# Performance work log

Hardware: AMD Instinct MI355X
Metric: run time of the kernel (lower is better)

## Reference

```python
import jax, jax.numpy as jnp
import numpy as np

B = 64
D_IN = 4000            # reduced from hardcoded 40000 to fit memory budget (see notes)
N_NODES = 200
ADJ = N_NODES * N_NODES  # 40000 entries per adjacency
E_PER = ADJ // 4         # strictly > 0.75-quantile of 40000 continuous values == top 10000
NEG_SLOPE = 0.2          # GATv2Conv default leaky_relu slope
LN_EPS = 1e-5


def _gelu(x):
    return jax.nn.gelu(x, approximate=False)  # torch F.gelu default = exact erf


def _gatv2(x, src, dst, valid, Wl, bl, Wr, br, att, bias, heads, ch, concat, n):
    # PyG GATv2Conv (share_weights=False): xl = lin_l(x), xr = lin_r(x)
    xl = (x @ Wl + bl).reshape(n, heads, ch)
    xr = (x @ Wr + br).reshape(n, heads, ch)
    e = jax.nn.leaky_relu(xl[src] + xr[dst], NEG_SLOPE)        # [E,H,C]
    logits = jnp.einsum('ehc,hc->eh', e, att)                   # [E,H]
    if valid is not None:
        logits = jnp.where(valid[:, None], logits, -jnp.inf)
    m = jax.ops.segment_max(logits, dst, num_segments=n)
    m = jnp.where(jnp.isfinite(m), m, 0.0)
    ex = jnp.exp(logits - m[dst])
    if valid is not None:
        ex = jnp.where(valid[:, None], ex, 0.0)
    denom = jax.ops.segment_sum(ex, dst, num_segments=n)
    alpha = ex / (denom[dst] + 1e-16)                            # scatter-softmax per target
    out = jax.ops.segment_sum(xl[src] * alpha[..., None], dst, num_segments=n)
    out = out.reshape(n, heads * ch) if concat else out.mean(axis=1)
    return out + bias


def _forward(raw_fc, gbW, gbb, feW1, feb1, feW2, feb2, ln_g, ln_b,
             W1l, b1l, W1r, b1r, att1, bias1,
             W2l, b2l, W2r, b2r, att2, bias2,
             W3l, b3l, W3r, b3r, att3, bias3):
    b = raw_fc.shape[0]
    n = b * N_NODES
    # ---- build_graph ----
    adj = jax.nn.sigmoid(raw_fc @ gbW + gbb).reshape(b, N_NODES, N_NODES)
    adj = (adj + jnp.swapaxes(adj, 1, 2)) * 0.5
    means = adj.mean(axis=2)                    # [B,200]
    stds = jnp.std(adj, axis=2, ddof=1) + 1e-6  # torch std is unbiased
    base = jnp.stack([means, stds], axis=-1).reshape(n, 2)
    h = _gelu(base @ feW1 + feb1) @ feW2 + feb2
    mu = h.mean(-1, keepdims=True)
    var = h.var(-1, keepdims=True)
    x = (h - mu) / jnp.sqrt(var + LN_EPS) * ln_g + ln_b          # LayerNorm(16)
    _, idx = jax.lax.top_k(adj.reshape(b, ADJ), E_PER)           # [B, 10000]
    row = idx // N_NODES
    col = idx % N_NODES
    offs = (jnp.arange(b) * N_NODES)[:, None]
    src = (row + offs).reshape(-1)
    dst = (col + offs).reshape(-1)
    # ---- GAT stack (eval mode: dropout = identity) ----
    x = _gelu(_gatv2(x, src, dst, None, W1l, b1l, W1r, b1r, att1, bias1, 8, 128, True, n))
    # layers 2/3 have add_self_loops=True: remove existing self loops, append one per node
    loops = jnp.arange(n)
    src2 = jnp.concatenate([src, loops])
    dst2 = jnp.concatenate([dst, loops])
    valid2 = jnp.concatenate([src != dst, jnp.ones((n,), bool)])
    x = _gelu(_gatv2(x, src2, dst2, valid2, W2l, b2l, W2r, b2r, att2, bias2, 4, 256, True, n))
    x = _gelu(_gatv2(x, src2, dst2, valid2, W3l, b3l, W3r, b3r, att3, bias3, 1, 512, False, n))
    # global_mean_pool: exactly 200 nodes per graph, contiguous ordering
    return x.reshape(b, N_NODES, 512).mean(axis=1)


def setup_inputs() -> dict:
    key = jax.random.key(0)
    ks = jax.random.split(key, 16)
    f32 = jnp.float32
    def gl(k, shape, fan_in):
        return jax.random.normal(k, shape, f32) / np.sqrt(fan_in)
    inp = {}
    inp['raw_fc'] = jax.random.normal(ks[0], (B, D_IN), f32)
    inp['gbW'] = gl(ks[1], (D_IN, ADJ), D_IN)
    inp['gbb'] = jnp.zeros((ADJ,), f32)
    inp['feW1'] = gl(ks[2], (2, 8), 2);      inp['feb1'] = jnp.zeros((8,), f32)
    inp['feW2'] = gl(ks[3], (8, 16), 8);     inp['feb2'] = jnp.zeros((16,), f32)
    inp['ln_g'] = jnp.ones((16,), f32);      inp['ln_b'] = jnp.zeros((16,), f32)
    inp['W1l'] = gl(ks[4], (16, 8 * 128), 16);   inp['b1l'] = jnp.zeros((8 * 128,), f32)
    inp['W1r'] = gl(ks[5], (16, 8 * 128), 16);   inp['b1r'] = jnp.zeros((8 * 128,), f32)
    inp['att1'] = gl(ks[6], (8, 128), 128);      inp['bias1'] = jnp.zeros((8 * 128,), f32)
    inp['W2l'] = gl(ks[7], (1024, 4 * 256), 1024); inp['b2l'] = jnp.zeros((4 * 256,), f32)
    inp['W2r'] = gl(ks[8], (1024, 4 * 256), 1024); inp['b2r'] = jnp.zeros((4 * 256,), f32)
    inp['att2'] = gl(ks[9], (4, 256), 256);        inp['bias2'] = jnp.zeros((4 * 256,), f32)
    inp['W3l'] = gl(ks[10], (1024, 512), 1024);    inp['b3l'] = jnp.zeros((512,), f32)
    inp['W3r'] = gl(ks[11], (1024, 512), 1024);    inp['b3r'] = jnp.zeros((512,), f32)
    inp['att3'] = gl(ks[12], (1, 512), 512);       inp['bias3'] = jnp.zeros((512,), f32)
    return inp


def reference(raw_fc, gbW, gbb, feW1, feb1, feW2, feb2, ln_g, ln_b,
              W1l, b1l, W1r, b1r, att1, bias1,
              W2l, b2l, W2r, b2r, att2, bias2,
              W3l, b3l, W3r, b3r, att3, bias3):
    return _forward(raw_fc, gbW, gbb, feW1, feb1, feW2, feb2, ln_g, ln_b,
                    W1l, b1l, W1r, b1r, att1, bias1,
                    W2l, b2l, W2r, b2r, att2, bias2,
                    W3l, b3l, W3r, b3r, att3, bias3)
```

## Files before the change

### kernel.cpp

```cpp
#include <hip/hip_runtime.h>
#include <hip/hip_fp16.h>
#include <math.h>
#include <cstdint>
#include <cstddef>

#define NGRAPH 64
#define NN 200
#define ADJN 40000
#define DIN 4000
#define NNODE 12800

typedef float    f32x4 __attribute__((ext_vector_type(4)));
typedef _Float16 f16x8 __attribute__((ext_vector_type(8)));
typedef _Float16 f16x4 __attribute__((ext_vector_type(4)));
typedef _Float16 f16x2 __attribute__((ext_vector_type(2)));
typedef short    bf8v  __attribute__((ext_vector_type(8)));
typedef short    bf4v  __attribute__((ext_vector_type(4)));

union BF8U  { bf8v v; bf4v h[2]; };
union F16X8U{ f16x8 v; f16x4 h[2]; f16x2 p[4]; };

__device__ __forceinline__ unsigned short f2bf(float f) {
  unsigned u = __float_as_uint(f);
  return (unsigned short)((u + 0x7fffu + ((u >> 16) & 1u)) >> 16);
}
__device__ __forceinline__ float bf2f(unsigned short s) {
  return __uint_as_float(((unsigned)s) << 16);
}
__device__ __forceinline__ float gelu_f(float x) {
  return x * 0.5f * (1.0f + erff(x * 0.70710678118654752f));
}

#if defined(__has_builtin)
#if __has_builtin(__builtin_amdgcn_fdot2)
#define FDOT2(a, b, c) __builtin_amdgcn_fdot2((a), (b), (c), false)
#endif
#endif
#ifndef FDOT2
#define FDOT2(a, b, c) ((c) + (float)(a)[0] * (float)(b)[0] + (float)(a)[1] * (float)(b)[1])
#endif

__device__ __forceinline__ void glds16(const _Float16* g, _Float16* l) {
  __builtin_amdgcn_global_load_lds(
      (const __attribute__((address_space(1))) void*)g,
      (__attribute__((address_space(3))) void*)l, 16, 0, 0);
}

__global__ __launch_bounds__(256) void prep_A(const float* __restrict__ A,
                                              short* __restrict__ Ahi,
                                              short* __restrict__ Alo) {
  const int i = blockIdx.x * 256 + threadIdx.x;
  const float v = A[i];
  const unsigned short h = f2bf(v);
  Ahi[i] = (short)h;
  Alo[i] = (short)f2bf(v - bf2f(h));
}

__global__ __launch_bounds__(256) void transp_all(
    const float* __restrict__ W2l, const float* __restrict__ W2r,
    const float* __restrict__ W3l, const float* __restrict__ W3r,
    _Float16* __restrict__ T2l, _Float16* __restrict__ T2r,
    _Float16* __restrict__ T3l, _Float16* __restrict__ T3r) {
  __shared__ float tile[32][33];
  const int z = blockIdx.z;
  if (z >= 2 && blockIdx.y >= 16) return;
  const float* src = (z == 0) ? W2l : (z == 1) ? W2r : (z == 2) ? W3l : W3r;
  _Float16* dst = (z == 0) ? T2l : (z == 1) ? T2r : (z == 2) ? T3l : T3r;
  const int N = (z < 2) ? 1024 : 512;
  const int K = 1024;
  const int bk = blockIdx.x * 32, bn = blockIdx.y * 32;
  const int tx = threadIdx.x & 31, ty = threadIdx.x >> 5;
#pragma unroll
  for (int r = 0; r < 32; r += 8) tile[ty + r][tx] = src[(size_t)(bk + ty + r) * N + bn + tx];
  __syncthreads();
#pragma unroll
  for (int r = 0; r < 32; r += 8)
    dst[(size_t)(bn + ty + r) * K + bk + tx] = (_Float16)tile[tx][ty + r];
}

#define BA_LOADW(WV, K0)                                                        \
  _Pragma("unroll") for (int q = 0; q < 8; ++q)                                 \
    WV[q] = W[(size_t)((K0) + kgrp * 8 + q) * ADJN + n0 + nn];

#define BA_CONV(PB, WV)                                                         \
  { bf4v h0, h1, l0, l1;                                                        \
    _Pragma("unroll") for (int i = 0; i < 4; ++i) {                             \
      unsigned short hh = (unsigned short)(__float_as_uint(WV[i]) >> 16);       \
      h0[i] = (short)hh;                                                        \
      l0[i] = (short)f2bf(WV[i] - bf2f(hh));                                    \
    }                                                                           \
    _Pragma("unroll") for (int i = 0; i < 4; ++i) {                             \
      unsigned short hh = (unsigned short)(__float_as_uint(WV[4 + i]) >> 16);   \
      h1[i] = (short)hh;                                                        \
      l1[i] = (short)f2bf(WV[4 + i] - bf2f(hh));                                \
    }                                                                           \
    *(bf4v*)(Wh[PB] + nn * 44 + kgrp * 8)     = h0;                             \
    *(bf4v*)(Wh[PB] + nn * 44 + kgrp * 8 + 4) = h1;                             \
    *(bf4v*)(Wl[PB] + nn * 44 + kgrp * 8)     = l0;                             \
    *(bf4v*)(Wl[PB] + nn * 44 + kgrp * 8 + 4) = l1;                             \
  }

#define BA_MFMA(PB, AHC, ALC)                                                   \
  _Pragma("unroll") for (int j = 0; j < 4; ++j) {                               \
    const int bc = (j * 16 + (lane & 15)) * 44 + kb;                            \
    BF8U bh, bl;                                                                \
    bh.h[0] = *(const bf4v*)(Wh[PB] + bc);                                      \
    bh.h[1] = *(const bf4v*)(Wh[PB] + bc + 4);                                  \
    bl.h[0] = *(const bf4v*)(Wl[PB] + bc);                                      \
    bl.h[1] = *(const bf4v*)(Wl[PB] + bc + 4);                                  \
    acc[j] = __builtin_amdgcn_mfma_f32_16x16x32_bf16(AHC, bh.v, acc[j], 0, 0, 0); \
    acc[j] = __builtin_amdgcn_mfma_f32_16x16x32_bf16(AHC, bl.v, acc[j], 0, 0, 0); \
    acc[j] = __builtin_amdgcn_mfma_f32_16x16x32_bf16(ALC, bh.v, acc[j], 0, 0, 0); \
  }

#define BA_LOADA(AH, AL, K0)                                                    \
  AH = *(const bf8v*)(Ahi + (size_t)arow * DIN + (K0) + kb);                    \
  AL = *(const bf8v*)(Alo + (size_t)arow * DIN + (K0) + kb);

__global__ __launch_bounds__(256) void build_adj(
    const short* __restrict__ Ahi, const short* __restrict__ Alo,
    const float* __restrict__ W, const float* __restrict__ bias,
    float* __restrict__ adj) {
  __shared__ short Wh[2][64 * 44], Wl[2][64 * 44];
  const int t = threadIdx.x, wave = t >> 6, lane = t & 63;
  const int n0 = blockIdx.x * 64;
  const int nn = t & 63, kgrp = t >> 6;
  const int kb = (lane >> 4) * 8;
  const int arow = wave * 16 + (lane & 15);
  f32x4 acc[4] = {};
  float wva[8], wvb[8];
  bf8v ahs0, als0, ahs1, als1;
  BA_LOADW(wva, 0)
  BA_LOADA(ahs0, als0, 0)
  BA_LOADW(wvb, 32)
  BA_LOADA(ahs1, als1, 32)
  BA_CONV(0, wva)
  for (int it = 0; it < 124; it += 2) {
    __syncthreads();
    {
      const bf8v ahc = ahs0, alc = als0;
      if (it + 2 < 125) {
        const int k2 = (it + 2) * 32;
        BA_LOADW(wva, k2)
        BA_LOADA(ahs0, als0, k2)
      }
      BA_MFMA(0, ahc, alc)
      BA_CONV(1, wvb)
    }
    __syncthreads();
    {
      const bf8v ahc = ahs1, alc = als1;
      if (it + 3 < 125) {
        const int k2 = (it + 3) * 32;
        BA_LOADW(wvb, k2)
        BA_LOADA(ahs1, als1, k2)
      }
      BA_MFMA(1, ahc, alc)
      if (it + 2 < 125) BA_CONV(0, wva)
    }
  }
  __syncthreads();
  BA_MFMA(0, ahs0, als0)
#pragma unroll
  for (int j = 0; j < 4; ++j) {
    const int col = n0 + j * 16 + (lane & 15);
    const float bb = bias[col];
#pragma unroll
    for (int vv = 0; vv < 4; ++vv) {
      const int row = wave * 16 + (lane >> 4) * 4 + vv;
      float x = acc[j][vv] + bb;
      adj[(size_t)row * ADJN + col] = 1.0f / (1.0f + __expf(-x));
    }
  }
}

__global__ __launch_bounds__(256) void symmetrize(const float* __restrict__ adj,
                                                  float* __restrict__ adjS) {
  __shared__ float tl[64][65];
  const int g = blockIdx.x;
  const int i0 = (blockIdx.y >> 2) * 64, j0 = (blockIdx.y & 3) * 64;
  const int tx = threadIdx.x & 63, ty = threadIdx.x >> 6;
  const float* ag = adj + (size_t)g * ADJN;
#pragma unroll
  for (int r = 0; r < 64; r += 4) {
    const int jr = j0 + ty + r;
    tl[ty + r][tx] = (jr < NN && i0 + tx < NN) ? ag[jr * NN + i0 + tx] : 0.f;
  }
  __syncthreads();
#pragma unroll
  for (int r = 0; r < 64; r += 4) {
    const int i = i0 + ty + r, j = j0 + tx;
    if (i < NN && j < NN)
      adjS[(size_t)g * ADJN + i * NN + j] = 0.5f * (ag[i * NN + j] + tl[tx][ty + r]);
  }
}

__global__ __launch_bounds__(256) void rowstats(const float* __restrict__ adjS,
                                                float* __restrict__ meanv,
                                                float* __restrict__ stdv) {
  const int row = blockIdx.x * 4 + (threadIdx.x >> 6);
  const int lane = threadIdx.x & 63;
  const float* r = adjS + (size_t)row * NN;
  float s = 0.f, q = 0.f;
#pragma unroll
  for (int k = 0; k < 4; ++k) {
    int i = k * 64 + lane;
    if (i < NN) { float v = r[i]; s += v; q += v * v; }
  }
#pragma unroll
  for (int off = 32; off > 0; off >>= 1) { s += __shfl_xor(s, off); q += __shfl_xor(q, off); }
  if (lane == 0) {
    float m = s * (1.0f / 200.0f);
    float var = (q - 200.0f * m * m) * (1.0f / 199.0f);
    var = fmaxf(var, 0.f);
    meanv[row] = m;
    stdv[row] = sqrtf(var) + 1e-6f;
  }
}

__global__ __launch_bounds__(1024) void radix_lists(
    const float* __restrict__ adjS,
    int* __restrict__ cnt1, int* __restrict__ cnt2,
    unsigned char* __restrict__ list1, unsigned char* __restrict__ list2) {
  __shared__ unsigned hist[4 * 2048];
  __shared__ unsigned s_pref, s_cA;
  const int g = blockIdx.x, t = threadIdx.x, lane = t & 63, wave = t >> 6;
  const float* v = adjS + (size_t)g * ADJN;
  unsigned prefix = 0, pmask = 0, cA = 0;
  const int shifts[3] = {20, 9, 0};
  const int widths[3] = {2048, 2048, 512};
  for (int pass = 0; pass < 3; ++pass) {
    const int nb = widths[pass], sh = shifts[pass];
    for (int i = t; i < 8192; i += 1024) hist[i] = 0u;
    __syncthreads();
    const int cpy = (lane & 3) * 2048;
    for (int e = t; e < ADJN; e += 1024) {
      unsigned u = __float_as_uint(v[e]);
      if ((u & pmask) == prefix) atomicAdd(&hist[cpy + ((u >> sh) & (nb - 1))], 1u);
    }
    __syncthreads();
    if (t < 64) {
      const int CH = nb >> 6;
      unsigned lsum = 0;
      for (int i = 0; i < CH; ++i) {
        const int b = t * CH + i;
        lsum += hist[b] + hist[2048 + b] + hist[4096 + b] + hist[6144 + b];
      }
      unsigned s = lsum;
#pragma unroll
      for (int off = 1; off < 64; off <<= 1) {
        unsigned o = __shfl_down(s, off);
        if (lane + off < 64) s += o;
      }
      const unsigned need = 10000u - cA;
      unsigned sn = __shfl_down(s, 1);
      const unsigned snext = (lane == 63) ? 0u : sn;
      if (s >= need && snext < need) {
        unsigned cum = snext;
        int bsel = t * CH;
        for (int i = CH - 1; i >= 0; --i) {
          const int b = t * CH + i;
          unsigned hb = hist[b] + hist[2048 + b] + hist[4096 + b] + hist[6144 + b];
          if (cum + hb >= need) { bsel = b; break; }
          cum += hb;
        }
        s_pref = prefix | ((unsigned)bsel << sh);
        s_cA = cA + cum;
      }
    }
    __syncthreads();
    prefix = s_pref; cA = s_cA;
    pmask |= (unsigned)(widths[pass] - 1) << sh;
    __syncthreads();
  }
  const float tv = __uint_as_float(prefix);
  for (int j = wave; j < NN; j += 16) {
    const float* row = adjS + (size_t)g * ADJN + (size_t)j * NN;
    unsigned char* l1 = list1 + ((size_t)g * NN + j) * NN;
    unsigned char* l2 = list2 + ((size_t)g * NN + j) * NN;
    int c1 = 0, c2 = 0;
#pragma unroll
    for (int r = 0; r < 4; ++r) {
      int i = r * 64 + lane;
      bool p1 = false, p2 = false;
      if (i < NN) { float vv = row[i]; p1 = (vv >= tv); p2 = p1 && (i != j); }
      unsigned long long b1 = __ballot(p1);
      unsigned long long b2 = __ballot(p2);
      unsigned long long below = (lane == 0) ? 0ull : ((~0ull) >> (64 - lane));
      if (p1) l1[c1 + __popcll(b1 & below)] = (unsigned char)i;
      if (p2) l2[c2 + __popcll(b2 & below)] = (unsigned char)i;
      c1 += (int)__popcll(b1); c2 += (int)__popcll(b2);
    }
    if (lane == 0) {
      l2[c2] = (unsigned char)j;
      cnt1[g * NN + j] = c1;
      cnt2[g * NN + j] = c2 + 1;
    }
  }
}

__global__ __launch_bounds__(256) void lin16_fused(
    const float* __restrict__ meanv, const float* __restrict__ stdv,
    const float* __restrict__ feW1, const float* __restrict__ feb1,
    const float* __restrict__ feW2, const float* __restrict__ feb2,
    const float* __restrict__ ln_g, const float* __restrict__ ln_b,
    const float* __restrict__ Wl, const float* __restrict__ bl,
    const float* __restrict__ Wr, const float* __restrict__ br,
    _Float16* __restrict__ outl, _Float16* __restrict__ outr) {
  __shared__ _Float16 Wt[1024 * 20];
  __shared__ float x0s[16][17];
  const int t = threadIdx.x, wave = t >> 6, lane = t & 63;
  const int mbase = blockIdx.x * 16;
  {
    const int n = t >> 4, o = t & 15;
    const float mu = meanv[mbase + n], sd = stdv[mbase + n];
    float h1[8];
#pragma unroll
    for (int k = 0; k < 8; ++k) h1[k] = gelu_f(mu * feW1[k] + sd * feW1[8 + k] + feb1[k]);
    float h2 = feb2[o];
#pragma unroll
    for (int k = 0; k < 8; ++k) h2 += h1[k] * feW2[k * 16 + o];
    float s = h2;
#pragma unroll
    for (int off = 1; off < 16; off <<= 1) s += __shfl_xor(s, off);
    s *= (1.0f / 16.0f);
    const float d = h2 - s;
    float vv = d * d;
#pragma unroll
    for (int off = 1; off < 16; off <<= 1) vv += __shfl_xor(vv, off);
    vv *= (1.0f / 16.0f);
    x0s[n][o] = d * (1.0f / sqrtf(vv + 1e-5f)) * ln_g[o] + ln_b[o];
  }
  __syncthreads();
  const int mrow = lane & 15, kg = lane >> 4;
  F16X8U af;
#pragma unroll
  for (int q = 0; q < 8; ++q) af.v[q] = (_Float16)0.f;
  if (kg < 2) {
#pragma unroll
    for (int q = 0; q < 8; ++q) af.v[q] = (_Float16)x0s[mrow][kg * 8 + q];
  }
#pragma unroll
  for (int mat = 0; mat < 2; ++mat) {
    if (mat) __syncthreads();
    const float* Wsrc = mat ? Wr : Wl;
    for (int i = t; i < 4096; i += 256) {
      const int k = i >> 8, n4 = (i & 255) * 4;
      float4 wv = *(const float4*)(Wsrc + (size_t)k * 1024 + n4);
      Wt[(n4 + 0) * 20 + k] = (_Float16)wv.x;
      Wt[(n4 + 1) * 20 + k] = (_Float16)wv.y;
      Wt[(n4 + 2) * 20 + k] = (_Float16)wv.z;
      Wt[(n4 + 3) * 20 + k] = (_Float16)wv.w;
    }
    __syncthreads();
    const float* bias = mat ? br : bl;
    _Float16* out = mat ? outr : outl;
#pragma unroll
    for (int nt = 0; nt < 16; ++nt) {
      const int n0 = wave * 256 + nt * 16;
      F16X8U bfv;
#pragma unroll
      for (int q = 0; q < 8; ++q) bfv.v[q] = (_Float16)0.f;
      if (kg < 2) bfv.v = *(const f16x8*)(Wt + (n0 + mrow) * 20 + kg * 8);
      f32x4 acc = {};
      acc = __builtin_amdgcn_mfma_f32_16x16x32_f16(af.v, bfv.v, acc, 0, 0, 0);
      const int col = n0 + mrow;
      const float bb = bias[col];
#pragma unroll
      for (int j = 0; j < 4; ++j)
        out[(size_t)(mbase + kg * 4 + j) * 1024 + col] = (_Float16)(acc[j] + bb);
    }
  }
}

__global__ __launch_bounds__(256, 2) void gemm_nt(
    const _Float16* __restrict__ A,
    const _Float16* __restrict__ Bt0, const _Float16* __restrict__ Bt1,
    const float* __restrict__ b0, const float* __restrict__ b1,
    _Float16* __restrict__ out0, _Float16* __restrict__ out1,
    int Nhalf, int tilesPerHalf) {
  __shared__ _Float16 As[2][128 * 64];
  __shared__ _Float16 Bs[2][128 * 64];
  const int mbase = blockIdx.y * 128;
  const int hsel = blockIdx.x / tilesPerHalf;
  const int ncol0 = (blockIdx.x % tilesPerHalf) * 128;
  const _Float16* Bt = hsel ? Bt1 : Bt0;
  const float* bias = hsel ? b1 : b0;
  _Float16* out = hsel ? out1 : out0;
  const int t = threadIdx.x, wave = t >> 6, lane = t & 63;
  const int wm = wave >> 1, wn = wave & 1;
  f32x4 acc[4][4] = {};
  const int srow = lane >> 3;
  const int sg = (lane & 7) ^ srow;
#pragma unroll
  for (int c = 0; c < 4; ++c) {
    const int rbase = wave * 32 + c * 8;
    glds16(A + (size_t)(mbase + rbase + srow) * 1024 + sg * 8, As[0] + rbase * 64);
    glds16(Bt + (size_t)(ncol0 + rbase + srow) * 1024 + sg * 8, Bs[0] + rbase * 64);
  }
  __syncthreads();
  for (int kt = 0; kt < 16; ++kt) {
    const int p = kt & 1;
    if (kt < 15) {
      const int k0 = (kt + 1) * 64;
#pragma unroll
      for (int c = 0; c < 4; ++c) {
        const int rbase = wave * 32 + c * 8;
        glds16(A + (size_t)(mbase + rbase + srow) * 1024 + k0 + sg * 8, As[p ^ 1] + rbase * 64);
        glds16(Bt + (size_t)(ncol0 + rbase + srow) * 1024 + k0 + sg * 8, Bs[p ^ 1] + rbase * 64);
      }
    }
#pragma unroll
    for (int ks = 0; ks < 2; ++ks) {
      F16X8U af[4], bfv[4];
#pragma unroll
      for (int m = 0; m < 4; ++m) {
        const int row = wm * 64 + m * 16 + (lane & 15);
        const int kk = ks * 32 + (lane >> 4) * 8;
        af[m].v = *(const f16x8*)(As[p] + row * 64 + (kk ^ ((row & 7) << 3)));
      }
#pragma unroll
      for (int j = 0; j < 4; ++j) {
        const int row = wn * 64 + j * 16 + (lane & 15);
        const int kk = ks * 32 + (lane >> 4) * 8;
        bfv[j].v = *(const f16x8*)(Bs[p] + row * 64 + (kk ^ ((row & 7) << 3)));
      }
#pragma unroll
      for (int j = 0; j < 4; ++j)
#pragma unroll
        for (int m = 0; m < 4; ++m)
          acc[m][j] = __builtin_amdgcn_mfma_f32_16x16x32_f16(af[m].v, bfv[j].v, acc[m][j], 0, 0, 0);
    }
    __syncthreads();
  }
#pragma unroll
  for (int j = 0; j < 4; ++j) {
    const int col = ncol0 + wn * 64 + j * 16 + (lane & 15);
    const float bb = bias[col];
#pragma unroll
    for (int m = 0; m < 4; ++m) {
#pragma unroll
      for (int vv = 0; vv < 4; ++vv) {
        const int row = mbase + wm * 64 + m * 16 + (lane >> 4) * 4 + vv;
        out[(size_t)row * Nhalf + col] = (_Float16)(acc[m][j][vv] + bb);
      }
    }
  }
}

template <int C, int HC, bool USE_LL>
__global__ __launch_bounds__(1024, 4) void gat_layer(
    const _Float16* __restrict__ xlb, const _Float16* __restrict__ xrb,
    const float* __restrict__ attw, const float* __restrict__ biasw,
    const int* __restrict__ cnts, const unsigned char* __restrict__ lists,
    _Float16* __restrict__ outb) {
  extern __shared__ char smem[];
  constexpr int XLB = 200 * C * 2;
  constexpr int XRW = 16 * C * 2;
  _Float16* xr_s = (_Float16*)(smem + XLB);
  _Float16* aw = (_Float16*)(smem + XLB + XRW);
  unsigned char* ll = (unsigned char*)(smem + XLB + XRW + 6400);
  unsigned* att_s = (unsigned*)(smem + XLB + XRW + 6400 + (USE_LL ? 3200 : 0));
  const int g = blockIdx.x;
  const int hd = blockIdx.y;
  const int t = threadIdx.x, wave = t >> 6, lane = t & 63;
  constexpr int GRP = (C == 128) ? 16 : 32;
  constexpr int NG = 64 / GRP;
  const int grp = lane / GRP, li = lane % GRP;

  for (int ch = t; ch < 200 * (C / 8); ch += 1024) {
    const int node = ch / (C / 8), cc = (ch % (C / 8)) * 8;
    f16x8 v = *(const f16x8*)(xlb + (size_t)(g * 200 + node) * HC + hd * C + cc);
    *(f16x8*)(smem + (((node * C + cc) * 2) ^ ((node & 15) << 4))) = v;
  }
  for (int i = t; i < C / 2; i += 1024) {
    f16x2 a;
    a[0] = (_Float16)attw[hd * C + 2 * i];
    a[1] = (_Float16)attw[hd * C + 2 * i + 1];
    att_s[i] = __builtin_bit_cast(unsigned, a);
  }
  __syncthreads();

  _Float16* xr_w = xr_s + wave * C;
  f16x8 xrreg;
  if (lane < C / 8)
    xrreg = *(const f16x8*)(xrb + (size_t)(g * 200 + wave) * HC + hd * C + lane * 8);

  for (int jj = wave; jj < 200; jj += 16) {
    const int gn = g * 200 + jj;
    const int cnt = cnts[gn];
    const unsigned char* lst = lists + (size_t)gn * NN;
    if (lane < C / 8) {
      *(f16x8*)(xr_w + lane * 8) = xrreg;
      if (jj + 16 < 200)
        xrreg = *(const f16x8*)(xrb + (size_t)(gn + 16) * HC + hd * C + lane * 8);
    }
    float lg[4] = {-INFINITY, -INFINITY, -INFINITY, -INFINITY};
#pragma unroll
    for (int r = 0; r < 4; ++r) {
      const int e = (r << 6) + lane;
      if (e < cnt) {
        const int s = lst[e];
        if constexpr (USE_LL) ll[wave * 200 + e] = (unsigned char)s;
        const int swz = (s & 15) << 4;
        float accv[4] = {0.f, 0.f, 0.f, 0.f};
#pragma unroll
        for (int c0 = 0; c0 < C; c0 += 16) {
          const int ai = ((c0 >> 4) & 1) * 2;
          const unsigned* ap = att_s + c0 / 2;
          F16X8U xa, xb, raa, rbb;
          xa.v = *(const f16x8*)(smem + (((s * C + c0) * 2) ^ swz));
          xb.v = *(const f16x8*)(smem + (((s * C + c0 + 8) * 2) ^ swz));
          raa.v = *(const f16x8*)(xr_w + c0);
          rbb.v = *(const f16x8*)(xr_w + c0 + 8);
#pragma unroll
          for (int pq = 0; pq < 4; ++pq) {
            f16x2 z = xa.p[pq] + raa.p[pq];
            f16x2 zs = z * (_Float16)0.2f;
            f16x2 m = __builtin_elementwise_max(z, zs);
            accv[ai] = FDOT2(__builtin_bit_cast(f16x2, ap[pq]), m, accv[ai]);
            f16x2 z2 = xb.p[pq] + rbb.p[pq];
            f16x2 zs2 = z2 * (_Float16)0.2f;
            f16x2 m2 = __builtin_elementwise_max(z2, zs2);
            accv[ai + 1] = FDOT2(__builtin_bit_cast(f16x2, ap[4 + pq]), m2, accv[ai + 1]);
          }
        }
        lg[r] = (accv[0] + accv[1]) + (accv[2] + accv[3]);
      }
    }
    float mloc = fmaxf(fmaxf(lg[0], lg[1]), fmaxf(lg[2], lg[3]));
#pragma unroll
    for (int off = 32; off > 0; off >>= 1) mloc = fmaxf(mloc, __shfl_xor(mloc, off));
    float ex[4]; float ps = 0.f;
#pragma unroll
    for (int r = 0; r < 4; ++r) { ex[r] = __expf(lg[r] - mloc); ps += ex[r]; }
#pragma unroll
    for (int off = 32; off > 0; off >>= 1) ps += __shfl_xor(ps, off);
    const float denom = ps + 1e-16f;
#pragma unroll
    for (int r = 0; r < 4; ++r) {
      const int e = (r << 6) + lane;
      if (e < cnt) aw[wave * 200 + e] = (_Float16)(ex[r] / denom);
    }
    float o[8] = {};
    for (int e0 = 0; e0 < cnt; e0 += NG) {
      const int e = e0 + grp;
      if (e < cnt) {
        const float a = (float)aw[wave * 200 + e];
        int s;
        if constexpr (USE_LL) s = ll[wave * 200 + e]; else s = lst[e];
        const int swz = (s & 15) << 4;
        f16x8 xv = *(const f16x8*)(smem + (((s * C + li * 8) * 2) ^ swz));
#pragma unroll
        for (int q = 0; q < 8; ++q) o[q] += a * (float)xv[q];
      }
    }
#pragma unroll
    for (int q = 0; q < 8; ++q) {
      if constexpr (GRP == 16) o[q] += __shfl_xor(o[q], 16);
      o[q] += __shfl_xor(o[q], 32);
    }
    if (grp == 0) {
      const int colb = hd * C + li * 8;
      f16x8 ov;
#pragma unroll
      for (int q = 0; q < 8; ++q) ov[q] = (_Float16)gelu_f(o[q] + biasw[colb + q]);
      *(f16x8*)(outb + (size_t)gn * HC + colb) = ov;
    }
  }
}

__global__ __launch_bounds__(1024, 4) void gat_l3(
    const _Float16* __restrict__ xlb, const _Float16* __restrict__ xrb,
    const float* __restrict__ attw, const float* __restrict__ biasw,
    const int* __restrict__ cnts, const unsigned char* __restrict__ lists,
    float* __restrict__ psum) {
  extern __shared__ char smem[];
  _Float16* xr_s = (_Float16*)(smem + 51200);
  float* plog = (float*)(smem + 64000);
  unsigned* att_s = (unsigned*)(smem + 104000);
  const int g = blockIdx.x, range = blockIdx.y, r0 = range * 50;
  const int t = threadIdx.x, wave = t >> 6, lane = t & 63;
  const int grp = lane >> 4, li = lane & 15;

  for (int chunk = 0; chunk < 4; ++chunk) {
    if (chunk) __syncthreads();
    for (int ch = t; ch < 200 * 16; ch += 1024) {
      const int node = ch >> 4, cc = (ch & 15) * 8;
      *(f16x8*)(smem + (((node * 128 + cc) * 2) ^ ((node & 15) << 4))) =
          *(const f16x8*)(xlb + (size_t)(g * 200 + node) * 512 + chunk * 128 + cc);
    }
    for (int ch = t; ch < 50 * 16; ch += 1024) {
      const int node = ch >> 4, cc = (ch & 15) * 8;
      *(f16x8*)(xr_s + node * 128 + cc) =
          *(const f16x8*)(xrb + (size_t)(g * 200 + r0 + node) * 512 + chunk * 128 + cc);
    }
    for (int i = t; i < 64; i += 1024) {
      f16x2 a;
      a[0] = (_Float16)attw[chunk * 128 + 2 * i];
      a[1] = (_Float16)attw[chunk * 128 + 2 * i + 1];
      att_s[i] = __builtin_bit_cast(unsigned, a);
    }
    __syncthreads();
    for (int jj = wave; jj < 50; jj += 16) {
      const int gn = g * 200 + r0 + jj;
      const int cnt = cnts[gn];
      const unsigned char* lst = lists + (size_t)gn * NN;
#pragma unroll
      for (int r = 0; r < 4; ++r) {
        const int e = (r << 6) + lane;
        if (e < cnt) {
          const int s = lst[e];
          const int swz = (s & 15) << 4;
          float accv[4] = {0.f, 0.f, 0.f, 0.f};
#pragma unroll
          for (int c0 = 0; c0 < 128; c0 += 16) {
            const int ai = ((c0 >> 4) & 1) * 2;
            const unsigned* ap = att_s + c0 / 2;
            F16X8U xa, xb, raa, rbb;
            xa.v = *(const f16x8*)(smem + (((s * 128 + c0) * 2) ^ swz));
            xb.v = *(const f16x8*)(smem + (((s * 128 + c0 + 8) * 2) ^ swz));
            raa.v = *(const f16x8*)(xr_s + jj * 128 + c0);
            rbb.v = *(const f16x8*)(xr_s + jj * 128 + c0 + 8);
#pragma unroll
            for (int pq = 0; pq < 4; ++pq) {
              f16x2 z = xa.p[pq] + raa.p[pq];
              f16x2 zs = z * (_Float16)0.2f;
              f16x2 m = __builtin_elementwise_max(z, zs);
              accv[ai] = FDOT2(__builtin_bit_cast(f16x2, ap[pq]), m, accv[ai]);
              f16x2 z2 = xb.p[pq] + rbb.p[pq];
              f16x2 zs2 = z2 * (_Float16)0.2f;
              f16x2 m2 = __builtin_elementwise_max(z2, zs2);
              accv[ai + 1] = FDOT2(__builtin_bit_cast(f16x2, ap[4 + pq]), m2, accv[ai + 1]);
            }
          }
          const float acc = (accv[0] + accv[1]) + (accv[2] + accv[3]);
          if (chunk == 0) plog[jj * 200 + e] = acc;
          else plog[jj * 200 + e] += acc;
        }
      }
    }
  }
  __syncthreads();
  for (int jj = wave; jj < 50; jj += 16) {
    const int gn = g * 200 + r0 + jj;
    const int cnt = cnts[gn];
    float lg[4] = {-INFINITY, -INFINITY, -INFINITY, -INFINITY};
#pragma unroll
    for (int r = 0; r < 4; ++r) {
      const int e = (r << 6) + lane;
      if (e < cnt) lg[r] = plog[jj * 200 + e];
    }
    float mloc = fmaxf(fmaxf(lg[0], lg[1]), fmaxf(lg[2], lg[3]));
#pragma unroll
    for (int off = 32; off > 0; off >>= 1) mloc = fmaxf(mloc, __shfl_xor(mloc, off));
    float ex[4]; float ps = 0.f;
#pragma unroll
    for (int r = 0; r < 4; ++r) { ex[r] = __expf(lg[r] - mloc); ps += ex[r]; }
#pragma unroll
    for (int off = 32; off > 0; off >>= 1) ps += __shfl_xor(ps, off);
    const float denom = ps + 1e-16f;
#pragma unroll
    for (int r = 0; r < 4; ++r) {
      const int e = (r << 6) + lane;
      if (e < cnt) plog[jj * 200 + e] = ex[r] / denom;
    }
  }
  for (int chunk = 0; chunk < 4; ++chunk) {
    __syncthreads();
    for (int ch = t; ch < 200 * 16; ch += 1024) {
      const int node = ch >> 4, cc = (ch & 15) * 8;
      *(f16x8*)(smem + (((node * 128 + cc) * 2) ^ ((node & 15) << 4))) =
          *(const f16x8*)(xlb + (size_t)(g * 200 + node) * 512 + chunk * 128 + cc);
    }
    __syncthreads();
    float p[8] = {};
    for (int jj = wave; jj < 50; jj += 16) {
      const int gn = g * 200 + r0 + jj;
      const int cnt = cnts[gn];
      const unsigned char* lst = lists + (size_t)gn * NN;
      float o[8] = {};
      for (int e0 = 0; e0 < cnt; e0 += 4) {
        const int e = e0 + grp;
        if (e < cnt) {
          const float a = plog[jj * 200 + e];
          const int s = lst[e];
          const int swz = (s & 15) << 4;
          f16x8 xv = *(const f16x8*)(smem + (((s * 128 + li * 8) * 2) ^ swz));
#pragma unroll
          for (int q = 0; q < 8; ++q) o[q] += a * (float)xv[q];
        }
      }
#pragma unroll
      for (int q = 0; q < 8; ++q) {
        o[q] += __shfl_xor(o[q], 16);
        o[q] += __shfl_xor(o[q], 32);
      }
      if (grp == 0) {
        const int colb = chunk * 128 + li * 8;
#pragma unroll
        for (int q = 0; q < 8; ++q) p[q] += gelu_f(o[q] + biasw[colb + q]);
      }
    }
    if (grp == 0) {
      const int slot = range * 16 + wave;
      float* pd = psum + ((size_t)slot * 64 + g) * 512 + chunk * 128 + li * 8;
      float4 a0 = {p[0], p[1], p[2], p[3]};
      float4 a1 = {p[4], p[5], p[6], p[7]};
      *(float4*)pd = a0;
      *(float4*)(pd + 4) = a1;
    }
  }
}

__global__ void finalize(const float* __restrict__ psum, float* __restrict__ out) {
  const int idx = blockIdx.x * 256 + threadIdx.x;
  float s = 0.f;
#pragma unroll
  for (int k = 0; k < 64; ++k) s += psum[(size_t)k * 32768 + idx];
  out[idx] = s * 0.005f;
}

extern "C" void kernel_launch(void* const* d_in, const int* in_sizes, int n_in,
                              void* d_out, int out_size, void* d_ws, size_t ws_size,
                              hipStream_t stream) {
  const float* raw_fc = (const float*)d_in[0];
  const float* gbW = (const float*)d_in[1];
  const float* gbb = (const float*)d_in[2];
  const float* feW1 = (const float*)d_in[3];
  const float* feb1 = (const float*)d_in[4];
  const float* feW2 = (const float*)d_in[5];
  const float* feb2 = (const float*)d_in[6];
  const float* ln_g = (const float*)d_in[7];
  const float* ln_b = (const float*)d_in[8];
  const float* W1l = (const float*)d_in[9];  const float* b1l = (const float*)d_in[10];
  const float* W1r = (const float*)d_in[11]; const float* b1r = (const float*)d_in[12];
  const float* att1 = (const float*)d_in[13]; const float* bias1 = (const float*)d_in[14];
  const float* W2l = (const float*)d_in[15]; const float* b2l = (const float*)d_in[16];
  const float* W2r = (const float*)d_in[17]; const float* b2r = (const float*)d_in[18];
  const float* att2 = (const float*)d_in[19]; const float* bias2 = (const float*)d_in[20];
  const float* W3l = (const float*)d_in[21]; const float* b3l = (const float*)d_in[22];
  const float* W3r = (const float*)d_in[23]; const float* b3r = (const float*)d_in[24];
  const float* att3 = (const float*)d_in[25]; const float* bias3 = (const float*)d_in[26];

  if (ws_size < 121000000) return;

  char* w = (char*)d_ws;
  float* adj   = (float*)(w + 0);
  float* adjS  = (float*)(w + 10240000);
  float* meanv = (float*)(w + 20480000);
  float* stdv  = (float*)(w + 20531200);
  int* cnt1    = (int*)(w + 21401856);
  int* cnt2    = (int*)(w + 21453056);
  unsigned char* list1 = (unsigned char*)(w + 21504256);
  unsigned char* list2 = (unsigned char*)(w + 24064256);
  _Float16* bufA = (_Float16*)(w + 26624256);
  _Float16* bufB = (_Float16*)(w + 52838656);
  _Float16* bufC = (_Float16*)(w + 79053056);
  float* psum = (float*)(w + 105267456);
  short* Ahi  = (short*)(w + 113656064);
  short* Alo  = (short*)(w + 114168064);
  _Float16* Wt2l = (_Float16*)(w + 114680064);
  _Float16* Wt2r = (_Float16*)(w + 116777216);
  _Float16* Wt3l = (_Float16*)(w + 118874368);
  _Float16* Wt3r = (_Float16*)(w + 119922944);

  const int SMEM_L1 = 65152;
  const int SMEM_L2 = 117504;
  const int SMEM_L3 = 104256;
  hipFuncSetAttribute((const void*)gat_layer<128, 1024, true>,
                      hipFuncAttributeMaxDynamicSharedMemorySize, SMEM_L1);
  hipFuncSetAttribute((const void*)gat_layer<256, 1024, false>,
                      hipFuncAttributeMaxDynamicSharedMemorySize, SMEM_L2);
  hipFuncSetAttribute((const void*)gat_l3,
                      hipFuncAttributeMaxDynamicSharedMemorySize, SMEM_L3);

  prep_A<<<1000, 256, 0, stream>>>(raw_fc, Ahi, Alo);
  transp_all<<<dim3(32, 32, 4), 256, 0, stream>>>(W2l, W2r, W3l, W3r, Wt2l, Wt2r, Wt3l, Wt3r);
  build_adj<<<625, 256, 0, stream>>>(Ahi, Alo, gbW, gbb, adj);
  symmetrize<<<dim3(64, 16), 256, 0, stream>>>(adj, adjS);
  rowstats<<<3200, 256, 0, stream>>>(adjS, meanv, stdv);
  radix_lists<<<64, 1024, 0, stream>>>(adjS, cnt1, cnt2, list1, list2);
  lin16_fused<<<800, 256, 0, stream>>>(meanv, stdv, feW1, feb1, feW2, feb2, ln_g, ln_b,
                                       W1l, b1l, W1r, b1r, bufA, bufB);
  gat_layer<128, 1024, true><<<dim3(64, 8), 1024, SMEM_L1, stream>>>(
      bufA, bufB, att1, bias1, cnt1, list1, bufC);
  gemm_nt<<<dim3(16, 100), 256, 0, stream>>>(bufC, Wt2l, Wt2r, b2l, b2r, bufA, bufB, 1024, 8);
  gat_layer<256, 1024, false><<<dim3(64, 4), 1024, SMEM_L2, stream>>>(
      bufA, bufB, att2, bias2, cnt2, list2, bufC);
  gemm_nt<<<dim3(8, 100), 256, 0, stream>>>(bufC, Wt3l, Wt3r, b3l, b3r, bufA, bufB, 512, 4);
  gat_l3<<<dim3(64, 4), 1024, SMEM_L3, stream>>>(bufA, bufB, att3, bias3, cnt2, list2, psum);
  finalize<<<128, 256, 0, stream>>>(psum, (float*)d_out);
}
```

Baseline: 968.9 us.

## Replace XOR swizzle with per-lane rotated column order and pack alpha with source index

```diff
diff --git a/kernel.cpp b/kernel.cpp
--- a/kernel.cpp
+++ b/kernel.cpp
@@ -19,6 +19,7 @@
 
 union BF8U  { bf8v v; bf4v h[2]; };
 union F16X8U{ f16x8 v; f16x4 h[2]; f16x2 p[4]; };
+union U4F   { uint4 u; unsigned w[4]; };
 
 __device__ __forceinline__ unsigned short f2bf(float f) {
   unsigned u = __float_as_uint(f);
@@ -448,7 +449,7 @@
   }
 }
 
-template <int C, int HC, bool USE_LL>
+template <int C, int HC>
 __global__ __launch_bounds__(1024, 4) void gat_layer(
     const _Float16* __restrict__ xlb, const _Float16* __restrict__ xrb,
     const float* __restrict__ attw, const float* __restrict__ biasw,
@@ -458,20 +459,21 @@
   constexpr int XLB = 200 * C * 2;
   constexpr int XRW = 16 * C * 2;
   _Float16* xr_s = (_Float16*)(smem + XLB);
-  _Float16* aw = (_Float16*)(smem + XLB + XRW);
-  unsigned char* ll = (unsigned char*)(smem + XLB + XRW + 6400);
-  unsigned* att_s = (unsigned*)(smem + XLB + XRW + 6400 + (USE_LL ? 3200 : 0));
+  unsigned* awp = (unsigned*)(smem + XLB + XRW);
+  unsigned* att_s = (unsigned*)(smem + XLB + XRW + 12800);
   const int g = blockIdx.x;
   const int hd = blockIdx.y;
   const int t = threadIdx.x, wave = t >> 6, lane = t & 63;
+  constexpr int NGR = C / 8;
   constexpr int GRP = (C == 128) ? 16 : 32;
   constexpr int NG = 64 / GRP;
   const int grp = lane / GRP, li = lane % GRP;
-
-  for (int ch = t; ch < 200 * (C / 8); ch += 1024) {
-    const int node = ch / (C / 8), cc = (ch % (C / 8)) * 8;
-    f16x8 v = *(const f16x8*)(xlb + (size_t)(g * 200 + node) * HC + hd * C + cc);
-    *(f16x8*)(smem + (((node * C + cc) * 2) ^ ((node & 15) << 4))) = v;
+  const int rc = lane & (NGR - 1) & 31;
+
+  for (int ch = t; ch < 200 * NGR; ch += 1024) {
+    const int node = ch / NGR, cc = (ch % NGR) * 8;
+    *(f16x8*)(smem + (node * C + cc) * 2) =
+        *(const f16x8*)(xlb + (size_t)(g * 200 + node) * HC + hd * C + cc);
   }
   for (int i = t; i < C / 2; i += 1024) {
     f16x2 a;
@@ -482,47 +484,44 @@
   __syncthreads();
 
   _Float16* xr_w = xr_s + wave * C;
+  const uint4* att4 = (const uint4*)att_s;
   f16x8 xrreg;
-  if (lane < C / 8)
+  if (lane < NGR)
     xrreg = *(const f16x8*)(xrb + (size_t)(g * 200 + wave) * HC + hd * C + lane * 8);
 
   for (int jj = wave; jj < 200; jj += 16) {
     const int gn = g * 200 + jj;
     const int cnt = cnts[gn];
     const unsigned char* lst = lists + (size_t)gn * NN;
-    if (lane < C / 8) {
+    if (lane < NGR) {
       *(f16x8*)(xr_w + lane * 8) = xrreg;
       if (jj + 16 < 200)
         xrreg = *(const f16x8*)(xrb + (size_t)(gn + 16) * HC + hd * C + lane * 8);
     }
     float lg[4] = {-INFINITY, -INFINITY, -INFINITY, -INFINITY};
+    int sreg[4];
 #pragma unroll
     for (int r = 0; r < 4; ++r) {
       const int e = (r << 6) + lane;
       if (e < cnt) {
         const int s = lst[e];
-        if constexpr (USE_LL) ll[wave * 200 + e] = (unsigned char)s;
-        const int swz = (s & 15) << 4;
+        sreg[r] = s;
+        const _Float16* xrow = (const _Float16*)(smem) + s * C;
         float accv[4] = {0.f, 0.f, 0.f, 0.f};
-#pragma unroll
-        for (int c0 = 0; c0 < C; c0 += 16) {
-          const int ai = ((c0 >> 4) & 1) * 2;
-          const unsigned* ap = att_s + c0 / 2;
-          F16X8U xa, xb, raa, rbb;
-          xa.v = *(const f16x8*)(smem + (((s * C + c0) * 2) ^ swz));
-          xb.v = *(const f16x8*)(smem + (((s * C + c0 + 8) * 2) ^ swz));
-          raa.v = *(const f16x8*)(xr_w + c0);
-          rbb.v = *(const f16x8*)(xr_w + c0 + 8);
+#pragma unroll 4
+        for (int gi0 = 0; gi0 < NGR; ++gi0) {
+          const int gi = (gi0 + rc) & (NGR - 1);
+          const int cc = gi * 8;
+          F16X8U xa, raa;
+          xa.v = *(const f16x8*)(xrow + cc);
+          raa.v = *(const f16x8*)(xr_w + cc);
+          U4F av; av.u = att4[gi];
 #pragma unroll
           for (int pq = 0; pq < 4; ++pq) {
             f16x2 z = xa.p[pq] + raa.p[pq];
             f16x2 zs = z * (_Float16)0.2f;
             f16x2 m = __builtin_elementwise_max(z, zs);
-            accv[ai] = FDOT2(__builtin_bit_cast(f16x2, ap[pq]), m, accv[ai]);
-            f16x2 z2 = xb.p[pq] + rbb.p[pq];
-            f16x2 zs2 = z2 * (_Float16)0.2f;
-            f16x2 m2 = __builtin_elementwise_max(z2, zs2);
-            accv[ai + 1] = FDOT2(__builtin_bit_cast(f16x2, ap[4 + pq]), m2, accv[ai + 1]);
+            accv[pq] = FDOT2(__builtin_bit_cast(f16x2, av.w[pq]), m, accv[pq]);
           }
         }
         lg[r] = (accv[0] + accv[1]) + (accv[2] + accv[3]);
@@ -540,17 +539,21 @@
 #pragma unroll
     for (int r = 0; r < 4; ++r) {
       const int e = (r << 6) + lane;
-      if (e < cnt) aw[wave * 200 + e] = (_Float16)(ex[r] / denom);
+      if (e < cnt) {
+        const unsigned short ab =
+            __builtin_bit_cast(unsigned short, (_Float16)(ex[r] / denom));
+        awp[wave * 200 + e] = ((unsigned)ab << 16) | (unsigned)sreg[r];
+      }
     }
     float o[8] = {};
     for (int e0 = 0; e0 < cnt; e0 += NG) {
       const int e = e0 + grp;
       if (e < cnt) {
-        const float a = (float)aw[wave * 200 + e];
-        int s;
-        if constexpr (USE_LL) s = ll[wave * 200 + e]; else s = lst[e];
-        const int swz = (s & 15) << 4;
-        f16x8 xv = *(const f16x8*)(smem + (((s * C + li * 8) * 2) ^ swz));
+        const unsigned v = awp[wave * 200 + e];
+        const int s = v & 0xFF;
+        const float a =
+            (float)__builtin_bit_cast(_Float16, (unsigned short)(v >> 16));
+        f16x8 xv = *(const f16x8*)((const _Float16*)smem + s * C + li * 8);
 #pragma unroll
         for (int q = 0; q < 8; ++q) o[q] += a * (float)xv[q];
       }
@@ -578,16 +581,19 @@
   extern __shared__ char smem[];
   _Float16* xr_s = (_Float16*)(smem + 51200);
   float* plog = (float*)(smem + 64000);
+  unsigned* plogp = (unsigned*)(smem + 64000);
   unsigned* att_s = (unsigned*)(smem + 104000);
   const int g = blockIdx.x, range = blockIdx.y, r0 = range * 50;
   const int t = threadIdx.x, wave = t >> 6, lane = t & 63;
   const int grp = lane >> 4, li = lane & 15;
+  const int rc = lane & 15;
+  const uint4* att4 = (const uint4*)att_s;
 
   for (int chunk = 0; chunk < 4; ++chunk) {
     if (chunk) __syncthreads();
     for (int ch = t; ch < 200 * 16; ch += 1024) {
       const int node = ch >> 4, cc = (ch & 15) * 8;
-      *(f16x8*)(smem + (((node * 128 + cc) * 2) ^ ((node & 15) << 4))) =
+      *(f16x8*)(smem + (node * 128 + cc) * 2) =
           *(const f16x8*)(xlb + (size_t)(g * 200 + node) * 512 + chunk * 128 + cc);
     }
     for (int ch = t; ch < 50 * 16; ch += 1024) {
@@ -611,27 +617,22 @@
         const int e = (r << 6) + lane;
         if (e < cnt) {
           const int s = lst[e];
-          const int swz = (s & 15) << 4;
+          const _Float16* xrow = (const _Float16*)(smem) + s * 128;
           float accv[4] = {0.f, 0.f, 0.f, 0.f};
-#pragma unroll
-          for (int c0 = 0; c0 < 128; c0 += 16) {
-            const int ai = ((c0 >> 4) & 1) * 2;
-            const unsigned* ap = att_s + c0 / 2;
-            F16X8U xa, xb, raa, rbb;
-            xa.v = *(const f16x8*)(smem + (((s * 128 + c0) * 2) ^ swz));
-            xb.v = *(const f16x8*)(smem + (((s * 128 + c0 + 8) * 2) ^ swz));
-            raa.v = *(const f16x8*)(xr_s + jj * 128 + c0);
-            rbb.v = *(const f16x8*)(xr_s + jj * 128 + c0 + 8);
+#pragma unroll 4
+          for (int gi0 = 0; gi0 < 16; ++gi0) {
+            const int gi = (gi0 + rc) & 15;
+            const int cc = gi * 8;
+            F16X8U xa, raa;
+            xa.v = *(const f16x8*)(xrow + cc);
+            raa.v = *(const f16x8*)(xr_s + jj * 128 + cc);
+            U4F av; av.u = att4[gi];
 #pragma unroll
             for (int pq = 0; pq < 4; ++pq) {
               f16x2 z = xa.p[pq] + raa.p[pq];
               f16x2 zs = z * (_Float16)0.2f;
               f16x2 m = __builtin_elementwise_max(z, zs);
-              accv[ai] = FDOT2(__builtin_bit_cast(f16x2, ap[pq]), m, accv[ai]);
-              f16x2 z2 = xb.p[pq] + rbb.p[pq];
-              f16x2 zs2 = z2 * (_Float16)0.2f;
-              f16x2 m2 = __builtin_elementwise_max(z2, zs2);
-              accv[ai + 1] = FDOT2(__builtin_bit_cast(f16x2, ap[4 + pq]), m2, accv[ai + 1]);
+              accv[pq] = FDOT2(__builtin_bit_cast(f16x2, av.w[pq]), m, accv[pq]);
             }
           }
           const float acc = (accv[0] + accv[1]) + (accv[2] + accv[3]);
@@ -645,6 +646,7 @@
   for (int jj = wave; jj < 50; jj += 16) {
     const int gn = g * 200 + r0 + jj;
     const int cnt = cnts[gn];
+    const unsigned char* lst = lists + (size_t)gn * NN;
     float lg[4] = {-INFINITY, -INFINITY, -INFINITY, -INFINITY};
 #pragma unroll
     for (int r = 0; r < 4; ++r) {
@@ -663,14 +665,18 @@
 #pragma unroll
     for (int r = 0; r < 4; ++r) {
       const int e = (r << 6) + lane;
-      if (e < cnt) plog[jj * 200 + e] = ex[r] / denom;
+      if (e < cnt) {
+        const unsigned short ab =
+            __builtin_bit_cast(unsigned short, (_Float16)(ex[r] / denom));
+        plogp[jj * 200 + e] = ((unsigned)ab << 16) | (unsigned)lst[e];
+      }
     }
   }
   for (int chunk = 0; chunk < 4; ++chunk) {
     __syncthreads();
     for (int ch = t; ch < 200 * 16; ch += 1024) {
       const int node = ch >> 4, cc = (ch & 15) * 8;
-      *(f16x8*)(smem + (((node * 128 + cc) * 2) ^ ((node & 15) << 4))) =
+      *(f16x8*)(smem + (node * 128 + cc) * 2) =
           *(const f16x8*)(xlb + (size_t)(g * 200 + node) * 512 + chunk * 128 + cc);
     }
     __syncthreads();
@@ -678,15 +684,15 @@
     for (int jj = wave; jj < 50; jj += 16) {
       const int gn = g * 200 + r0 + jj;
       const int cnt = cnts[gn];
-      const unsigned char* lst = lists + (size_t)gn * NN;
       float o[8] = {};
       for (int e0 = 0; e0 < cnt; e0 += 4) {
         const int e = e0 + grp;
         if (e < cnt) {
-          const float a = plog[jj * 200 + e];
-          const int s = lst[e];
-          const int swz = (s & 15) << 4;
-          f16x8 xv = *(const f16x8*)(smem + (((s * 128 + li * 8) * 2) ^ swz));
+          const unsigned v = plogp[jj * 200 + e];
+          const int s = v & 0xFF;
+          const float a =
+              (float)__builtin_bit_cast(_Float16, (unsigned short)(v >> 16));
+          f16x8 xv = *(const f16x8*)((const _Float16*)smem + s * 128 + li * 8);
 #pragma unroll
           for (int q = 0; q < 8; ++q) o[q] += a * (float)xv[q];
         }
@@ -765,12 +771,12 @@
   _Float16* Wt3l = (_Float16*)(w + 118874368);
   _Float16* Wt3r = (_Float16*)(w + 119922944);
 
-  const int SMEM_L1 = 65152;
-  const int SMEM_L2 = 117504;
+  const int SMEM_L1 = 68352;
+  const int SMEM_L2 = 123904;
   const int SMEM_L3 = 104256;
-  hipFuncSetAttribute((const void*)gat_layer<128, 1024, true>,
+  hipFuncSetAttribute((const void*)gat_layer<128, 1024>,
                       hipFuncAttributeMaxDynamicSharedMemorySize, SMEM_L1);
-  hipFuncSetAttribute((const void*)gat_layer<256, 1024, false>,
+  hipFuncSetAttribute((const void*)gat_layer<256, 1024>,
                       hipFuncAttributeMaxDynamicSharedMemorySize, SMEM_L2);
   hipFuncSetAttribute((const void*)gat_l3,
                       hipFuncAttributeMaxDynamicSharedMemorySize, SMEM_L3);
@@ -783,10 +789,10 @@
   radix_lists<<<64, 1024, 0, stream>>>(adjS, cnt1, cnt2, list1, list2);
   lin16_fused<<<800, 256, 0, stream>>>(meanv, stdv, feW1, feb1, feW2, feb2, ln_g, ln_b,
                                        W1l, b1l, W1r, b1r, bufA, bufB);
-  gat_layer<128, 1024, true><<<dim3(64, 8), 1024, SMEM_L1, stream>>>(
+  gat_layer<128, 1024><<<dim3(64, 8), 1024, SMEM_L1, stream>>>(
       bufA, bufB, att1, bias1, cnt1, list1, bufC);
   gemm_nt<<<dim3(16, 100), 256, 0, stream>>>(bufC, Wt2l, Wt2r, b2l, b2r, bufA, bufB, 1024, 8);
-  gat_layer<256, 1024, false><<<dim3(64, 4), 1024, SMEM_L2, stream>>>(
+  gat_layer<256, 1024><<<dim3(64, 4), 1024, SMEM_L2, stream>>>(
       bufA, bufB, att2, bias2, cnt2, list2, bufC);
   gemm_nt<<<dim3(8, 100), 256, 0, stream>>>(bufC, Wt3l, Wt3r, b3l, b3r, bufA, bufB, 512, 4);
   gat_l3<<<dim3(64, 4), 1024, SMEM_L3, stream>>>(bufA, bufB, att3, bias3, cnt2, list2, psum);
```

Measured after the change: 906.8 us. -6.4%, faster.
